# Optimization experiments

Measured on AMD Instinct MI355X. Metric: run time of the kernel, lower is better.

The kernel has to match this reference:

```python
import jax, jax.numpy as jnp
import numpy as np

NEG_SLOPE = 0.2
NEG_INF = -1e9


def _gat_branch(x, src, dst, edge_type, t, W, a_src, a_dst, b):
    """Single-head PyG GATConv restricted (by masking) to edges with edge_type == t,
    with self-loops added (PyG default add_self_loops=True)."""
    N = x.shape[0]
    h = x @ W                                   # [N, out_dim]
    s = h @ a_src                               # [N] source attention term
    d = h @ a_dst                               # [N] destination attention term
    # real edges (masked by type)
    e_edge = jax.nn.leaky_relu(s[src] + d[dst], NEG_SLOPE)
    e_edge = jnp.where(edge_type == t, e_edge, NEG_INF)
    # self-loop edges i -> i
    e_self = jax.nn.leaky_relu(s + d, NEG_SLOPE)
    dst_all = jnp.concatenate([dst, jnp.arange(N)])          # [E+N]
    e_all = jnp.concatenate([e_edge, e_self])                 # [E+N]
    # softmax over incoming edges per destination node (segment softmax)
    m = jax.ops.segment_max(e_all, dst_all, num_segments=N)
    p = jnp.exp(e_all - m[dst_all])
    denom = jax.ops.segment_sum(p, dst_all, num_segments=N)
    alpha = p / denom[dst_all]                                 # [E+N]
    msg = jnp.concatenate([h[src], h], axis=0) * alpha[:, None]
    return jax.ops.segment_sum(msg, dst_all, num_segments=N) + b


def setup_inputs() -> dict:
    key = jax.random.key(0)
    ks = jax.random.split(key, 12)
    N, E, in_dim, out_dim = 100000, 1000000, 64, 64
    glorot = (6.0 / (in_dim + out_dim)) ** 0.5
    att = (6.0 / (1 + out_dim)) ** 0.5
    return {
        "x": jax.random.normal(ks[0], (N, in_dim), dtype=jnp.float32),
        "edge_index": jax.random.randint(ks[1], (2, E), 0, N),
        "edge_type": jax.random.randint(ks[2], (E,), 0, 2),
        "W_login": jax.random.uniform(ks[3], (in_dim, out_dim), jnp.float32, -glorot, glorot),
        "a_src_login": jax.random.uniform(ks[4], (out_dim,), jnp.float32, -att, att),
        "a_dst_login": jax.random.uniform(ks[5], (out_dim,), jnp.float32, -att, att),
        "b_login": jnp.zeros((out_dim,), jnp.float32),
        "W_exec": jax.random.uniform(ks[6], (in_dim, out_dim), jnp.float32, -glorot, glorot),
        "a_src_exec": jax.random.uniform(ks[7], (out_dim,), jnp.float32, -att, att),
        "a_dst_exec": jax.random.uniform(ks[8], (out_dim,), jnp.float32, -att, att),
        "b_exec": jnp.zeros((out_dim,), jnp.float32),
    }


def reference(x, edge_index, edge_type, W_login, a_src_login, a_dst_login, b_login,
              W_exec, a_src_exec, a_dst_exec, b_exec):
    src, dst = edge_index[0], edge_index[1]
    out = _gat_branch(x, src, dst, edge_type, 0, W_login, a_src_login, a_dst_login, b_login)
    out = out + _gat_branch(x, src, dst, edge_type, 1, W_exec, a_src_exec, a_dst_exec, b_exec)
    return out
```

## Files before the change

kernel.cpp:

```cpp
#include <hip/hip_runtime.h>

#define D 64
#define CAP 896
#define BINB 256
#define GEMMB 768
#define BINCH 1600

typedef unsigned short u16;
typedef __attribute__((ext_vector_type(8))) __bf16 bf16x8;
typedef __attribute__((ext_vector_type(4))) float f32x4;

__device__ __forceinline__ float lrelu(float x) { return x > 0.f ? x : 0.2f * x; }
__device__ __forceinline__ u16 f2bf(float f) {
    unsigned u = __float_as_uint(f);
    return (u16)((u + 0x7fffu + ((u >> 16) & 1u)) >> 16);
}
__device__ __forceinline__ unsigned pack2(float lo, float hi) {
    return (unsigned)f2bf(lo) | ((unsigned)f2bf(hi) << 16);
}
__device__ __forceinline__ float blo(unsigned u) { return __uint_as_float(u << 16); }
__device__ __forceinline__ float bhi(unsigned u) { return __uint_as_float(u & 0xffff0000u); }

struct SG { u16 Wb[2][64][64]; u16 Xb[64][72]; float wsd[4][64]; };
struct SB { int cnt[BINCH]; };

__global__ __launch_bounds__(256) void k_gb(
    const float* __restrict__ x,
    const float* __restrict__ W0, const float* __restrict__ as0, const float* __restrict__ ad0,
    const float* __restrict__ W1, const float* __restrict__ as1, const float* __restrict__ ad1,
    u16* __restrict__ hb, float* __restrict__ s_tab, float* __restrict__ d_tab,
    int N, int ntiles,
    const int* __restrict__ src, const int* __restrict__ dst, const int* __restrict__ et,
    int* __restrict__ bktcnt, unsigned* __restrict__ bkt, int E, int nbk, int Eseg)
{
    __shared__ union SM { SG g; SB bn; } sm;
    const int tid = threadIdx.x;

    if (blockIdx.x >= GEMMB) {
        int* cnt_l = sm.bn.cnt;
        const int blk = blockIdx.x - GEMMB;
        const long e0 = (long)blk * Eseg;
        const long e1 = min(e0 + (long)Eseg, (long)E);
        for (int base = 0; base < nbk; base += BINCH) {
            const int lim = min(BINCH, nbk - base);
            for (int i = tid; i < lim; i += 256) cnt_l[i] = 0;
            __syncthreads();
            long i = e0 + tid;
            for (; i + 256 * 7 < e1; i += 256 * 8) {
                int d8[8];
#pragma unroll
                for (int k = 0; k < 8; ++k) d8[k] = dst[i + 256 * k];
#pragma unroll
                for (int k = 0; k < 8; ++k) {
                    const int bb = (d8[k] >> 6) - base;
                    if ((unsigned)bb < (unsigned)lim) atomicAdd(&cnt_l[bb], 1);
                }
            }
            for (; i < e1; i += 256) {
                const int bb = (dst[i] >> 6) - base;
                if ((unsigned)bb < (unsigned)lim) atomicAdd(&cnt_l[bb], 1);
            }
            __syncthreads();
            for (int j = tid; j < lim; j += 256) {
                const int c = cnt_l[j];
                cnt_l[j] = c ? atomicAdd(bktcnt + base + j, c) : 0;
            }
            __syncthreads();
            i = e0 + tid;
            for (; i + 256 * 7 < e1; i += 256 * 8) {
                int d8[8], s8[8], t8[8];
#pragma unroll
                for (int k = 0; k < 8; ++k) d8[k] = dst[i + 256 * k];
#pragma unroll
                for (int k = 0; k < 8; ++k) s8[k] = src[i + 256 * k];
#pragma unroll
                for (int k = 0; k < 8; ++k) t8[k] = et[i + 256 * k];
#pragma unroll
                for (int k = 0; k < 8; ++k) {
                    const int bb = (d8[k] >> 6) - base;
                    if ((unsigned)bb < (unsigned)lim) {
                        const int slot = atomicAdd(&cnt_l[bb], 1);
                        if (slot < CAP)
                            bkt[(long)(base + bb) * CAP + slot] =
                                ((unsigned)(d8[k] & 63) << 18) | ((unsigned)s8[k] << 1) | (unsigned)t8[k];
                    }
                }
            }
            for (; i < e1; i += 256) {
                const int d = dst[i];
                const int bb = (d >> 6) - base;
                if ((unsigned)bb < (unsigned)lim) {
                    const int slot = atomicAdd(&cnt_l[bb], 1);
                    if (slot < CAP)
                        bkt[(long)(base + bb) * CAP + slot] =
                            ((unsigned)(d & 63) << 18) | ((unsigned)src[i] << 1) | (unsigned)et[i];
                }
            }
            __syncthreads();
        }
        return;
    }

    auto& Wb  = sm.g.Wb;
    auto& Xb  = sm.g.Xb;
    auto& wsd = sm.g.wsd;

    for (int i = tid; i < 4096; i += 256) {
        const int k = i >> 6, n = i & 63;
        Wb[0][n][k] = f2bf(W0[i]);
        Wb[1][n][k] = f2bf(W1[i]);
    }
    {
        const int k = tid & 63;
        const int v = tid >> 6;
        const float* Ws = (v < 2) ? W0 : W1;
        const float* av = (v == 0) ? as0 : (v == 1) ? ad0 : (v == 2) ? as1 : ad1;
        float q = 0.f;
        for (int n = 0; n < 64; ++n) q = fmaf(Ws[(k << 6) + n], av[n], q);
        wsd[v][k] = q;
    }
    __syncthreads();

    const int lane = tid & 63;
    const int nl = lane & 15, quad = lane >> 4;
    const int wv = tid >> 6;

    bf16x8 bfrag[2][4][2];
#pragma unroll
    for (int br = 0; br < 2; ++br)
#pragma unroll
        for (int t = 0; t < 4; ++t)
#pragma unroll
            for (int h = 0; h < 2; ++h)
                bfrag[br][t][h] = *(const bf16x8*)&Wb[br][t * 16 + nl][h * 32 + quad * 8];

    const int rstage = tid >> 2;
    const int kc = (tid & 3) << 4;

    for (int tile = blockIdx.x; tile < ntiles; tile += GEMMB) {
        const long n0 = (long)tile << 6;
        __syncthreads();
        {
            long row = n0 + rstage; if (row >= N) row = N - 1;
            const float4* xp = (const float4*)(x + row * D + kc);
            const float4 v0 = xp[0], v1 = xp[1], v2 = xp[2], v3 = xp[3];

            unsigned q[8];
            q[0] = pack2(v0.x, v0.y); q[1] = pack2(v0.z, v0.w);
            q[2] = pack2(v1.x, v1.y); q[3] = pack2(v1.z, v1.w);
            q[4] = pack2(v2.x, v2.y); q[5] = pack2(v2.z, v2.w);
            q[6] = pack2(v3.x, v3.y); q[7] = pack2(v3.z, v3.w);
            *(uint4*)&Xb[rstage][kc]     = make_uint4(q[0], q[1], q[2], q[3]);
            *(uint4*)&Xb[rstage][kc + 8] = make_uint4(q[4], q[5], q[6], q[7]);

            float ps[4];
#pragma unroll
            for (int v = 0; v < 4; ++v) {
                const float4* wp = (const float4*)&wsd[v][kc];
                const float4 wa = wp[0], wb = wp[1], wc = wp[2], wd = wp[3];
                float s = 0.f;
                s = fmaf(v0.x, wa.x, s); s = fmaf(v0.y, wa.y, s);
                s = fmaf(v0.z, wa.z, s); s = fmaf(v0.w, wa.w, s);
                s = fmaf(v1.x, wb.x, s); s = fmaf(v1.y, wb.y, s);
                s = fmaf(v1.z, wb.z, s); s = fmaf(v1.w, wb.w, s);
                s = fmaf(v2.x, wc.x, s); s = fmaf(v2.y, wc.y, s);
                s = fmaf(v2.z, wc.z, s); s = fmaf(v2.w, wc.w, s);
                s = fmaf(v3.x, wd.x, s); s = fmaf(v3.y, wd.y, s);
                s = fmaf(v3.z, wd.z, s); s = fmaf(v3.w, wd.w, s);
                ps[v] = s;
            }
#pragma unroll
            for (int v = 0; v < 4; ++v) {
                ps[v] += __shfl_xor(ps[v], 1, 64);
                ps[v] += __shfl_xor(ps[v], 2, 64);
            }
            const long rw = n0 + rstage;
            if ((tid & 3) == 0 && rw < N) {
                s_tab[(rw << 1)]     = ps[0]; d_tab[(rw << 1)]     = ps[1];
                s_tab[(rw << 1) | 1] = ps[2]; d_tab[(rw << 1) | 1] = ps[3];
            }
        }
        __syncthreads();

        const int rbase = wv << 4;
        const bf16x8 a0 = *(const bf16x8*)&Xb[rbase + nl][quad * 8];
        const bf16x8 a1 = *(const bf16x8*)&Xb[rbase + nl][32 + quad * 8];

        f32x4 acc[2][4];
#pragma unroll
        for (int br = 0; br < 2; ++br)
#pragma unroll
            for (int t = 0; t < 4; ++t) {
                f32x4 c = {0.f, 0.f, 0.f, 0.f};
                c = __builtin_amdgcn_mfma_f32_16x16x32_bf16(a0, bfrag[br][t][0], c, 0, 0, 0);
                c = __builtin_amdgcn_mfma_f32_16x16x32_bf16(a1, bfrag[br][t][1], c, 0, 0, 0);
                acc[br][t] = c;
            }

#pragma unroll
        for (int reg = 0; reg < 4; ++reg) {
            const long row = n0 + rbase + (quad << 2) + reg;
            if (row < N) {
#pragma unroll
                for (int br = 0; br < 2; ++br) {
                    uint2 v;
                    v.x = pack2(acc[br][0][reg], acc[br][1][reg]);
                    v.y = pack2(acc[br][2][reg], acc[br][3][reg]);
                    *(uint2*)(hb + (((row << 1) | br) << 6) + (nl << 2)) = v;
                }
            }
        }
    }
}

__global__ __launch_bounds__(512) void k_proc(
    const int* __restrict__ bktcnt, const unsigned* __restrict__ bkt,
    const float* __restrict__ s_tab, const float* __restrict__ d_tab,
    const u16* __restrict__ hb,
    const float* __restrict__ b0, const float* __restrict__ b1,
    float* __restrict__ out, int N)
{
    __shared__ uint2 tok2[CAP + 128];
    __shared__ int   degl[64];
    __shared__ int   curl[64];
    __shared__ float den[128];
    __shared__ float dl[128];
    __shared__ float bsum[64];

    const int tid = threadIdx.x;
    const int b = blockIdx.x;
    const int lo = b << 6;
    const int cnt_nodes = min(64, N - lo);
    const int nb = min(bktcnt[b], CAP);

    if (tid < 64) {
        degl[tid] = (lo + tid < N) ? 2 : 0;
        bsum[tid] = b0[tid] + b1[tid];
    }
    if (tid < 128) {
        den[tid] = 0.f;
        const int n = lo + (tid >> 1);
        dl[tid] = (n < N) ? d_tab[(n << 1) | (tid & 1)] : 0.f;
    }
    __syncthreads();

    unsigned pr[2]; int ns = 0;
    for (int i = tid; i < nb; i += 512) {
        const unsigned p = bkt[(long)b * CAP + i];
        pr[ns++] = p;
        atomicAdd(&degl[(p >> 18) & 63], 1);
    }
    __syncthreads();
    if (tid < 64) {
        int v = degl[tid];
        const int orig = v;
#pragma unroll
        for (int o = 1; o < 64; o <<= 1) {
            const int u = __shfl_up(v, o, 64);
            if (tid >= o) v += u;
        }
        curl[tid] = v - orig;
    }
    __syncthreads();
    if (tid < 2 * cnt_nodes) {
        const int ni = tid >> 1;
        const int slot = atomicAdd(&curl[ni], 1);
        tok2[slot].x = ((unsigned)ni << 18) | ((unsigned)((lo + ni) << 1)) | (unsigned)(tid & 1);
    }
    for (int k = 0, i = tid; k < ns; i += 512, ++k) {
        const unsigned p = pr[k];
        const int slot = atomicAdd(&curl[(p >> 18) & 63], 1);
        tok2[slot].x = p;
    }
    __syncthreads();

    const int T = nb + (cnt_nodes << 1);
    for (int j = tid; j < T; j += 512) {
        const unsigned u = tok2[j].x;
        const int idx = (int)(((u >> 18) << 1) | (u & 1u));
        const float e = lrelu(s_tab[u & 0x3FFFFu] + dl[idx]);
        const float p = __expf(e);
        tok2[j].y = __float_as_uint(p);
        atomicAdd(&den[idx], p);
    }
    __syncthreads();

    const int lane = tid & 63;
    const int wave = tid >> 6;
    const int q = lane >> 4;
    const int cl = lane & 15;

    for (int ni = wave; ni < cnt_nodes; ni += 8) {
        const int cnt = degl[ni];
        const int off = curl[ni] - cnt;
        const float r0 = 1.f / den[(ni << 1)];
        const float r1 = 1.f / den[(ni << 1) | 1];

        float4 acc = {0.f, 0.f, 0.f, 0.f};
        const int nq = (cnt + 3) >> 2;
        int pp = 0;
        for (; pp + 1 < nq; pp += 2) {
            const int iA = (pp << 2) + q;
            const int iB = iA + 4;
            const uint2 eA = tok2[off + iA];
            const uint2 eB = tok2[off + (iB < cnt ? iB : cnt - 1)];
            const float aA = __uint_as_float(eA.y) * ((eA.x & 1u) ? r1 : r0);
            float aB = __uint_as_float(eB.y) * ((eB.x & 1u) ? r1 : r0);
            if (iB >= cnt) aB = 0.f;
            const uint2 uA = *(const uint2*)(hb + ((long)(eA.x & 0x3FFFFu) << 6) + (cl << 2));
            const uint2 uB = *(const uint2*)(hb + ((long)(eB.x & 0x3FFFFu) << 6) + (cl << 2));
            acc.x = fmaf(aA, blo(uA.x), acc.x);
            acc.y = fmaf(aA, bhi(uA.x), acc.y);
            acc.z = fmaf(aA, blo(uA.y), acc.z);
            acc.w = fmaf(aA, bhi(uA.y), acc.w);
            acc.x = fmaf(aB, blo(uB.x), acc.x);
            acc.y = fmaf(aB, bhi(uB.x), acc.y);
            acc.z = fmaf(aB, blo(uB.y), acc.z);
            acc.w = fmaf(aB, bhi(uB.y), acc.w);
        }
        if (pp < nq) {
            const int iA = (pp << 2) + q;
            const uint2 eA = tok2[off + (iA < cnt ? iA : cnt - 1)];
            float aA = __uint_as_float(eA.y) * ((eA.x & 1u) ? r1 : r0);
            if (iA >= cnt) aA = 0.f;
            const uint2 uA = *(const uint2*)(hb + ((long)(eA.x & 0x3FFFFu) << 6) + (cl << 2));
            acc.x = fmaf(aA, blo(uA.x), acc.x);
            acc.y = fmaf(aA, bhi(uA.x), acc.y);
            acc.z = fmaf(aA, blo(uA.y), acc.z);
            acc.w = fmaf(aA, bhi(uA.y), acc.w);
        }
        acc.x += __shfl_xor(acc.x, 16, 64);
        acc.y += __shfl_xor(acc.y, 16, 64);
        acc.z += __shfl_xor(acc.z, 16, 64);
        acc.w += __shfl_xor(acc.w, 16, 64);
        acc.x += __shfl_xor(acc.x, 32, 64);
        acc.y += __shfl_xor(acc.y, 32, 64);
        acc.z += __shfl_xor(acc.z, 32, 64);
        acc.w += __shfl_xor(acc.w, 32, 64);
        if (lane < 16) {
            float* op = out + ((long)(lo + ni) << 6);
            op[cl]      = acc.x + bsum[cl];
            op[16 + cl] = acc.y + bsum[16 + cl];
            op[32 + cl] = acc.z + bsum[32 + cl];
            op[48 + cl] = acc.w + bsum[48 + cl];
        }
    }
}

extern "C" void kernel_launch(void* const* d_in, const int* in_sizes, int n_in,
                              void* d_out, int out_size, void* d_ws, size_t ws_size,
                              hipStream_t stream) {
    const float* x   = (const float*)d_in[0];
    const int*   ei  = (const int*)d_in[1];
    const int*   et  = (const int*)d_in[2];
    const float* W0  = (const float*)d_in[3];
    const float* as0 = (const float*)d_in[4];
    const float* ad0 = (const float*)d_in[5];
    const float* b0  = (const float*)d_in[6];
    const float* W1  = (const float*)d_in[7];
    const float* as1 = (const float*)d_in[8];
    const float* ad1 = (const float*)d_in[9];
    const float* b1  = (const float*)d_in[10];
    float* out = (float*)d_out;

    const int N = in_sizes[0] / D;
    const int E = in_sizes[1] / 2;
    const int* src = ei;
    const int* dst = ei + E;

    const int nbk = (N + 63) >> 6;

    char* w = (char*)d_ws;
    u16* hb = (u16*)w;            w += (size_t)2 * N * D * sizeof(u16);
    float* s_tab = (float*)w;     w += (size_t)2 * N * sizeof(float);
    float* d_tab = (float*)w;     w += (size_t)2 * N * sizeof(float);
    int* bktcnt = (int*)w;        w += (size_t)nbk * sizeof(int);
    unsigned* bkt = (unsigned*)w; w += (size_t)nbk * CAP * sizeof(unsigned);

    const int ntiles = (N + 63) / 64;
    const int Eseg = (E + BINB - 1) / BINB;

    hipMemsetAsync(bktcnt, 0, (size_t)nbk * sizeof(int), stream);
    k_gb<<<GEMMB + BINB, 256, 0, stream>>>(x, W0, as0, ad0, W1, as1, ad1,
                                           hb, s_tab, d_tab, N, ntiles,
                                           src, dst, et, bktcnt, bkt, E, nbk, Eseg);
    k_proc<<<nbk, 512, 0, stream>>>(bktcnt, bkt, s_tab, d_tab, hb, b0, b1, out, N);
}
```

Baseline: 180.4 us.

## Replace global atomic bucket allocation with per-block count matrix and offset scan

Measured after the change: 251.1 us. 39.2% more time.

```diff
diff --git a/kernel.cpp b/kernel.cpp
--- a/kernel.cpp
+++ b/kernel.cpp
@@ -2,7 +2,7 @@
 
 #define D 64
 #define CAP 896
-#define BINB 256
+#define CNTB 512
 #define GEMMB 768
 #define BINCH 1600
 
@@ -24,14 +24,13 @@
 struct SG { u16 Wb[2][64][64]; u16 Xb[64][72]; float wsd[4][64]; };
 struct SB { int cnt[BINCH]; };
 
-__global__ __launch_bounds__(256) void k_gb(
+__global__ __launch_bounds__(256) void k_gc(
     const float* __restrict__ x,
     const float* __restrict__ W0, const float* __restrict__ as0, const float* __restrict__ ad0,
     const float* __restrict__ W1, const float* __restrict__ as1, const float* __restrict__ ad1,
     u16* __restrict__ hb, float* __restrict__ s_tab, float* __restrict__ d_tab,
     int N, int ntiles,
-    const int* __restrict__ src, const int* __restrict__ dst, const int* __restrict__ et,
-    int* __restrict__ bktcnt, unsigned* __restrict__ bkt, int E, int nbk, int Eseg)
+    const int* __restrict__ dst, u16* __restrict__ cm, int E, int nbk, int Eseg)
 {
     __shared__ union SM { SG g; SB bn; } sm;
     const int tid = threadIdx.x;
@@ -61,41 +60,8 @@
                 if ((unsigned)bb < (unsigned)lim) atomicAdd(&cnt_l[bb], 1);
             }
             __syncthreads();
-            for (int j = tid; j < lim; j += 256) {
-                const int c = cnt_l[j];
-                cnt_l[j] = c ? atomicAdd(bktcnt + base + j, c) : 0;
-            }
-            __syncthreads();
-            i = e0 + tid;
-            for (; i + 256 * 7 < e1; i += 256 * 8) {
-                int d8[8], s8[8], t8[8];
-#pragma unroll
-                for (int k = 0; k < 8; ++k) d8[k] = dst[i + 256 * k];
-#pragma unroll
-                for (int k = 0; k < 8; ++k) s8[k] = src[i + 256 * k];
-#pragma unroll
-                for (int k = 0; k < 8; ++k) t8[k] = et[i + 256 * k];
-#pragma unroll
-                for (int k = 0; k < 8; ++k) {
-                    const int bb = (d8[k] >> 6) - base;
-                    if ((unsigned)bb < (unsigned)lim) {
-                        const int slot = atomicAdd(&cnt_l[bb], 1);
-                        if (slot < CAP)
-                            bkt[(long)(base + bb) * CAP + slot] =
-                                ((unsigned)(d8[k] & 63) << 18) | ((unsigned)s8[k] << 1) | (unsigned)t8[k];
-                    }
-                }
-            }
-            for (; i < e1; i += 256) {
-                const int d = dst[i];
-                const int bb = (d >> 6) - base;
-                if ((unsigned)bb < (unsigned)lim) {
-                    const int slot = atomicAdd(&cnt_l[bb], 1);
-                    if (slot < CAP)
-                        bkt[(long)(base + bb) * CAP + slot] =
-                            ((unsigned)(d & 63) << 18) | ((unsigned)src[i] << 1) | (unsigned)et[i];
-                }
-            }
+            for (int j = tid; j < lim; j += 256)
+                cm[(size_t)blk * nbk + base + j] = (u16)cnt_l[j];
             __syncthreads();
         }
         return;
@@ -210,6 +176,71 @@
                 }
             }
         }
+    }
+}
+
+__global__ __launch_bounds__(256) void k_off(
+    u16* __restrict__ cm, int* __restrict__ bktcnt, int nbk)
+{
+    const int j = blockIdx.x * 256 + threadIdx.x;
+    if (j >= nbk) return;
+    int run = 0;
+    for (int b = 0; b < CNTB; ++b) {
+        const u16 c = cm[(size_t)b * nbk + j];
+        cm[(size_t)b * nbk + j] = (u16)run;
+        run += c;
+    }
+    bktcnt[j] = run;
+}
+
+__global__ __launch_bounds__(256) void k_emit(
+    const int* __restrict__ src, const int* __restrict__ dst,
+    const int* __restrict__ et, const u16* __restrict__ cm,
+    unsigned* __restrict__ bkt, int E, int nbk, int Eseg)
+{
+    extern __shared__ int curl[];
+    const int tid = threadIdx.x;
+    const int blk = blockIdx.x;
+    const long e0 = (long)blk * Eseg;
+    const long e1 = min(e0 + (long)Eseg, (long)E);
+
+    for (int base = 0; base < nbk; base += BINCH) {
+        const int lim = min(BINCH, nbk - base);
+        for (int i = tid; i < lim; i += 256)
+            curl[i] = (int)cm[(size_t)blk * nbk + base + i];
+        __syncthreads();
+
+        long i = e0 + tid;
+        for (; i + 256 * 7 < e1; i += 256 * 8) {
+            int d8[8], s8[8], t8[8];
+#pragma unroll
+            for (int k = 0; k < 8; ++k) d8[k] = dst[i + 256 * k];
+#pragma unroll
+            for (int k = 0; k < 8; ++k) s8[k] = src[i + 256 * k];
+#pragma unroll
+            for (int k = 0; k < 8; ++k) t8[k] = et[i + 256 * k];
+#pragma unroll
+            for (int k = 0; k < 8; ++k) {
+                const int bb = (d8[k] >> 6) - base;
+                if ((unsigned)bb < (unsigned)lim) {
+                    const int slot = atomicAdd(&curl[bb], 1);
+                    if (slot < CAP)
+                        bkt[(long)(base + bb) * CAP + slot] =
+                            ((unsigned)(d8[k] & 63) << 18) | ((unsigned)s8[k] << 1) | (unsigned)t8[k];
+                }
+            }
+        }
+        for (; i < e1; i += 256) {
+            const int d = dst[i];
+            const int bb = (d >> 6) - base;
+            if ((unsigned)bb < (unsigned)lim) {
+                const int slot = atomicAdd(&curl[bb], 1);
+                if (slot < CAP)
+                    bkt[(long)(base + bb) * CAP + slot] =
+                        ((unsigned)(d & 63) << 18) | ((unsigned)src[i] << 1) | (unsigned)et[i];
+            }
+        }
+        __syncthreads();
     }
 }
 
@@ -376,13 +407,17 @@
     float* d_tab = (float*)w;     w += (size_t)2 * N * sizeof(float);
     int* bktcnt = (int*)w;        w += (size_t)nbk * sizeof(int);
     unsigned* bkt = (unsigned*)w; w += (size_t)nbk * CAP * sizeof(unsigned);
+    u16* cm = (u16*)w;            w += (size_t)CNTB * nbk * sizeof(u16);
 
     const int ntiles = (N + 63) / 64;
-    const int Eseg = (E + BINB - 1) / BINB;
-
-    hipMemsetAsync(bktcnt, 0, (size_t)nbk * sizeof(int), stream);
-    k_gb<<<GEMMB + BINB, 256, 0, stream>>>(x, W0, as0, ad0, W1, as1, ad1,
+    const int Eseg = (E + CNTB - 1) / CNTB;
+    const int offb = (nbk + 255) / 256;
+
+    k_gc<<<GEMMB + CNTB, 256, 0, stream>>>(x, W0, as0, ad0, W1, as1, ad1,
                                            hb, s_tab, d_tab, N, ntiles,
-                                           src, dst, et, bktcnt, bkt, E, nbk, Eseg);
+                                           dst, cm, E, nbk, Eseg);
+    k_off<<<offb, 256, 0, stream>>>(cm, bktcnt, nbk);
+    k_emit<<<CNTB, 256, (size_t)BINCH * sizeof(int), stream>>>(
+        src, dst, et, cm, bkt, E, nbk, Eseg);
     k_proc<<<nbk, 512, 0, stream>>>(bktcnt, bkt, s_tab, d_tab, hb, b0, b1, out, N);
 }
```
